# Optimization experiments

Hardware: AMD Instinct MI355X
Metric: run time of the kernel (lower is better)

## Reference

```python
import jax, jax.numpy as jnp
import numpy as np

C = 256
CK = C // 8  # key/query channels


def setup_inputs() -> dict:
    key = jax.random.key(0)
    ks = jax.random.split(key, 7)
    B, H, W = 8, 64, 64
    x = jax.random.normal(ks[0], (B, C, H, W), dtype=jnp.float32)
    # 1x1 conv weights (out_ch, in_ch) and biases. Spectral norm is a weight
    # reparameterization; at forward time it is just a conv with (normalized)
    # weights, so we sample weights directly.
    Wf = jax.random.normal(ks[1], (CK, C), dtype=jnp.float32) * 0.02
    bf = jnp.zeros((CK,), dtype=jnp.float32)
    Wg = jax.random.normal(ks[2], (CK, C), dtype=jnp.float32) * 0.02
    bg = jnp.zeros((CK,), dtype=jnp.float32)
    Wh = jax.random.normal(ks[3], (C, C), dtype=jnp.float32) * 0.02
    bh = jnp.zeros((C,), dtype=jnp.float32)
    gamma = jnp.ones((1,), dtype=jnp.float32) * 0.5  # nonzero so attention path matters
    return {"x": x, "Wf": Wf, "bf": bf, "Wg": Wg, "bg": bg, "Wh": Wh, "bh": bh, "gamma": gamma}


def reference(x, Wf, bf, Wg, bg, Wh, bh, gamma):
    b, c, h, w = x.shape
    n = h * w
    xf = x.reshape(b, c, n)  # [B, C, N]
    # 1x1 convs == per-pixel linear maps
    fx = jnp.einsum("kc,bcn->bkn", Wf, xf) + bf[None, :, None]  # [B, CK, N]
    gx = jnp.einsum("kc,bcn->bkn", Wg, xf) + bg[None, :, None]  # [B, CK, N]
    hx = jnp.einsum("oc,bcn->bon", Wh, xf) + bh[None, :, None]  # [B, C, N]
    # sx[b, i, j] = <fx[:, i], gx[:, j]>
    sx = jnp.einsum("bki,bkj->bij", fx, gx)  # [B, N, N]
    # torch F.softmax(sx, dim=1): normalize over the first N axis (i)
    beta = jax.nn.softmax(sx, axis=1)
    ox = jnp.einsum("bci,bij->bcj", hx, beta).reshape(b, c, h, w)
    return gamma.reshape(()) * ox + x
```

## Files before the change

kernel.cpp:

```cpp
#include <hip/hip_runtime.h>
#include <stdint.h>


typedef __bf16 bf16;
typedef __bf16 bf16x2 __attribute__((ext_vector_type(2)));
typedef __bf16 bf16x8 __attribute__((ext_vector_type(8)));
typedef float  f32x16 __attribute__((ext_vector_type(16)));
typedef float  f32x4  __attribute__((ext_vector_type(4)));
typedef unsigned char u8;
typedef long   i64;

#define BATCH 8
#define CC    256
#define CKK   32
#define NN    4096
#define LOG2E 1.4426950408889634f

__device__ __forceinline__ f32x16 zero16() {
  f32x16 z;
#pragma unroll
  for (int i = 0; i < 16; ++i) z[i] = 0.0f;
  return z;
}

__device__ __forceinline__ unsigned pack2(float lo, float hi) {
  bf16x2 v = {(bf16)lo, (bf16)hi};
  return __builtin_bit_cast(unsigned, v);
}

__device__ __forceinline__ f32x16 mfma32(bf16x8 a, bf16x8 b, f32x16 c) {
  return __builtin_amdgcn_mfma_f32_32x32x16_bf16(a, b, c, 0, 0, 0);
}

__device__ __forceinline__ f32x16 mfma8(i64 a, i64 b, f32x16 c) {
  return __builtin_amdgcn_mfma_f32_32x32x16_fp8_fp8(a, b, c, 0, 0, 0);
}

#define GLDS16(srcp, dstp)                                                         \
  __builtin_amdgcn_global_load_lds(                                               \
      (const __attribute__((address_space(1))) void*)(srcp),                      \
      (__attribute__((address_space(3))) void*)(dstp), 16, 0, 0)

__global__ __launch_bounds__(256) void k_transpose(const float* __restrict__ x,
                                                   bf16* __restrict__ xT) {
  __shared__ float tile[64][65];
  const int n0 = blockIdx.x * 64;
  const int c0 = blockIdx.y * 64;
  const int b  = blockIdx.z;
  const int t = threadIdx.x;
  const int tn = t & 63, trow = t >> 6;
#pragma unroll
  for (int i = 0; i < 16; ++i) {
    int c = trow + i * 4;
    tile[c][tn] = x[((size_t)(b * CC + c0 + c)) * NN + n0 + tn];
  }
  __syncthreads();
#pragma unroll
  for (int i = 0; i < 16; ++i) {
    int n = trow + i * 4;
    xT[((size_t)(b * NN + n0 + n)) * CC + c0 + tn] = (bf16)tile[tn][n];
  }
}

__global__ __launch_bounds__(64) void k_wprep(const float* __restrict__ Wf, const float* __restrict__ bfv,
                                              const float* __restrict__ Wg, const float* __restrict__ bg,
                                              const float* __restrict__ Wh, const float* __restrict__ bh,
                                              bf16* __restrict__ Wcat, float* __restrict__ bcat) {
  const int ko = blockIdx.x;
  const int t = threadIdx.x;
  const float* src;
  float scale = 1.0f;
  if (ko < 32) src = Wf + (size_t)ko * CC;
  else if (ko < 64) { src = Wg + (size_t)(ko - 32) * CC; scale = LOG2E; }
  else src = Wh + (size_t)(ko - 64) * CC;
#pragma unroll
  for (int i = 0; i < 4; ++i)
    Wcat[(size_t)ko * CC + t + i * 64] = (bf16)(src[t + i * 64] * scale);
  if (ko == 0) {
    for (int i = t; i < 320; i += 64) {
      float v = (i < 32) ? bfv[i] : (i < 64) ? bg[i - 32] * LOG2E : bh[i - 64];
      bcat[i] = v;
    }
  }
}

__global__ __launch_bounds__(256, 1) void k_proj(const bf16* __restrict__ xT,
                                                 const bf16* __restrict__ Wcat,
                                                 const float* __restrict__ bcat,
                                                 bf16* __restrict__ fxT, bf16* __restrict__ gxT,
                                                 u8* __restrict__ hx8) {
  const int d = blockIdx.x;
  const int b = d & 7, nb = d >> 3;
  const int t = threadIdx.x;
  const int w = t >> 6, ln = t & 63, ln31 = ln & 31, h = ln >> 5;
  const int n = nb * 128 + w * 32 + ln31;

  f32x16 acc[10];
#pragma unroll
  for (int mt = 0; mt < 10; ++mt) acc[mt] = zero16();

  const bf16* xrow = xT + ((size_t)(b * NN + n)) * CC;
#pragma unroll
  for (int ks = 0; ks < 16; ++ks) {
    bf16x8 bfrag = *(const bf16x8*)(xrow + ks * 16 + h * 8);
#pragma unroll
    for (int mt = 0; mt < 10; ++mt) {
      bf16x8 afrag = *(const bf16x8*)(Wcat + (size_t)(mt * 32 + ln31) * CC + ks * 16 + h * 8);
      acc[mt] = mfma32(afrag, bfrag, acc[mt]);
    }
  }

#pragma unroll
  for (int mt = 0; mt < 10; ++mt) {
#pragma unroll
    for (int q = 0; q < 4; ++q) {
      const int ko0 = mt * 32 + 8 * q + 4 * h;
      float v0 = acc[mt][4 * q + 0] + bcat[ko0 + 0];
      float v1 = acc[mt][4 * q + 1] + bcat[ko0 + 1];
      float v2 = acc[mt][4 * q + 2] + bcat[ko0 + 2];
      float v3 = acc[mt][4 * q + 3] + bcat[ko0 + 3];
      if (mt < 2) {
        bf16* dst = (mt == 0 ? fxT : gxT) + ((size_t)(b * NN + n)) * CKK + (8 * q + 4 * h);
        uint2 pv;
        pv.x = pack2(v0, v1);
        pv.y = pack2(v2, v3);
        *(uint2*)dst = pv;
      } else {
        const int c = ko0 - 64;
        unsigned wpk = (unsigned)__builtin_amdgcn_cvt_pk_fp8_f32(v0, v1, 0, false);
        wpk = (unsigned)__builtin_amdgcn_cvt_pk_fp8_f32(v2, v3, (int)wpk, true);
        u8* hp = hx8 + ((size_t)(b * CC + c)) * NN + n;
        hp[0]          = (u8)(wpk & 0xff);
        hp[NN]         = (u8)((wpk >> 8) & 0xff);
        hp[2 * NN]     = (u8)((wpk >> 16) & 0xff);
        hp[3 * NN]     = (u8)(wpk >> 24);
      }
    }
  }
}

__global__ __launch_bounds__(512, 2) void k_attn(const bf16* __restrict__ fxT,
                                                 const bf16* __restrict__ gxT,
                                                 const u8* __restrict__ hx8,
                                                 const float* __restrict__ x,
                                                 const float* __restrict__ gammap,
                                                 float* __restrict__ out) {
  extern __shared__ __align__(16) char smem[];
  __shared__ float lsh[128];
  const int d = blockIdx.x;
  const int b = d & 7, jb = d >> 3;
  const int t = threadIdx.x;
  const int g = t >> 8;
  const int tg = t & 255;
  const int wg = tg >> 6;
  const int ln = t & 63, ln31 = ln & 31, h = ln >> 5;
  const int j = jb * 128 + wg * 32 + ln31;
  const int kbase = g * 2048;

  const bf16* fxb = fxT + (size_t)b * NN * CKK;
  const u8*   hxb = hx8 + (size_t)b * CC * NN;

  u8*   vsg = (u8*)smem + g * 32768;
  bf16* ksg = (bf16*)(smem + 65536) + g * 6144;

  const bf16* qrow = gxT + ((size_t)b * NN + j) * CKK;
  bf16x8 qf0 = *(const bf16x8*)(qrow + h * 8);
  bf16x8 qf1 = *(const bf16x8*)(qrow + 16 + h * 8);
  asm volatile("" ::: "memory");

  int voff8[4];
#pragma unroll
  for (int ks = 0; ks < 4; ++ks)
    voff8[ks] = ln31 * 64 + (((ks + (ln31 >> 1)) & 3) * 16) + 8 * h;
  const int tk = (ln31 >> 1) & 3;
  const int ko0 = ln31 * 32 + ((h ^ tk) * 8);
  const int ko1 = ln31 * 32 + (((2 + h) ^ tk) * 8);

  const int vm = ((ln & 3) - (ln >> 3)) & 3;
  const u8* vlane8 = hxb + (size_t)(wg * 64 + (ln >> 2)) * NN + vm * 16;
  const int krow_l = ln >> 2;
  const int kcol_l = ((ln & 3) ^ ((ln >> 3) & 3)) * 8;
  const bf16* klane = fxb + (size_t)(wg * 16 + krow_l) * CKK + kcol_l;

#define STAGEV(slot, i0s)                                                     \
  {                                                                            \
    _Pragma("unroll")                                                          \
    for (int q = 0; q < 4; ++q)                                                \
      GLDS16(vlane8 + (size_t)q * 16 * NN + (i0s),                             \
             vsg + (slot) * 16384 + (wg * 4 + q) * 1024);                      \
  }
#define STAGEK(kslot, i0s)                                                    \
  { GLDS16(klane + (size_t)(i0s) * CKK, ksg + (kslot) * 2048 + wg * 16 * 32); }

  f32x16 oacc[8];
#pragma unroll
  for (int ct = 0; ct < 8; ++ct) oacc[ct] = zero16();
  float l_run = 0.0f;
  i64 pf[4] = {};

  auto QK = [&](int kslot, f32x16& s0, f32x16& s1) {
    const bf16* kt = ksg + kslot * 2048;
    bf16x8 kf00 = *(const bf16x8*)(kt + ko0);
    bf16x8 kf01 = *(const bf16x8*)(kt + ko1);
    bf16x8 kf10 = *(const bf16x8*)(kt + 1024 + ko0);
    bf16x8 kf11 = *(const bf16x8*)(kt + 1024 + ko1);
    s0 = zero16(); s1 = zero16();
    s0 = mfma32(kf00, qf0, s0);
    s0 = mfma32(kf01, qf1, s0);
    s1 = mfma32(kf10, qf0, s1);
    s1 = mfma32(kf11, qf1, s1);
  };
  auto SM = [&](const f32x16& s0, const f32x16& s1) {
    float e0[16], e1[16];
#pragma unroll
    for (int r = 0; r < 16; ++r) e0[r] = __builtin_exp2f(s0[r]);
#pragma unroll
    for (int r = 0; r < 16; ++r) e1[r] = __builtin_exp2f(s1[r]);
    float ls0 = 0.0f, ls1 = 0.0f, ls2 = 0.0f, ls3 = 0.0f;
#pragma unroll
    for (int r = 0; r < 4; ++r) {
      ls0 += e0[r];      ls1 += e0[4 + r];
      ls2 += e0[8 + r];  ls3 += e0[12 + r];
      ls0 += e1[r];      ls1 += e1[4 + r];
      ls2 += e1[8 + r];  ls3 += e1[12 + r];
    }
    l_run += (ls0 + ls1) + (ls2 + ls3);
    unsigned pk4[8];
#pragma unroll
    for (int A = 0; A < 4; ++A) {
      unsigned w = (unsigned)__builtin_amdgcn_cvt_pk_fp8_f32(e0[4 * A], e0[4 * A + 1], 0, false);
      pk4[A] = (unsigned)__builtin_amdgcn_cvt_pk_fp8_f32(e0[4 * A + 2], e0[4 * A + 3], (int)w, true);
    }
#pragma unroll
    for (int A = 0; A < 4; ++A) {
      unsigned w = (unsigned)__builtin_amdgcn_cvt_pk_fp8_f32(e1[4 * A], e1[4 * A + 1], 0, false);
      pk4[4 + A] = (unsigned)__builtin_amdgcn_cvt_pk_fp8_f32(e1[4 * A + 2], e1[4 * A + 3], (int)w, true);
    }
#pragma unroll
    for (int f = 0; f < 4; ++f) {
      unsigned xw = pk4[2 * f], yw = pk4[2 * f + 1];
      asm("v_permlane32_swap_b32 %0, %1" : "+v"(xw), "+v"(yw));
      pf[f] = (i64)(((unsigned long long)yw << 32) | xw);
    }
  };
  auto PV = [&](int slot) {
    const u8* vb = vsg + slot * 16384;
    i64 va0, va1, va2, va3, vn0, vn1, vn2, vn3;
    va0 = *(const i64*)(vb + voff8[0]);
    va1 = *(const i64*)(vb + voff8[1]);
    va2 = *(const i64*)(vb + voff8[2]);
    va3 = *(const i64*)(vb + voff8[3]);
    __builtin_amdgcn_s_setprio(1);
#pragma unroll
    for (int ct = 0; ct < 8; ++ct) {
      if (ct < 7) {
        const u8* vrow = vb + (ct + 1) * 2048;
        vn0 = *(const i64*)(vrow + voff8[0]);
        vn1 = *(const i64*)(vrow + voff8[1]);
        vn2 = *(const i64*)(vrow + voff8[2]);
        vn3 = *(const i64*)(vrow + voff8[3]);
      }
      oacc[ct] = mfma8(va0, pf[0], oacc[ct]);
      oacc[ct] = mfma8(va1, pf[1], oacc[ct]);
      oacc[ct] = mfma8(va2, pf[2], oacc[ct]);
      oacc[ct] = mfma8(va3, pf[3], oacc[ct]);
      va0 = vn0; va1 = vn1; va2 = vn2; va3 = vn3;
    }
    __builtin_amdgcn_s_setprio(0);
  };

  STAGEV(0, kbase);
  STAGEK(0, kbase);
  STAGEK(1, kbase + 64);

  for (int kb = 0; kb < 32; ++kb) {
    asm volatile("s_waitcnt vmcnt(0)" ::: "memory");
    __builtin_amdgcn_s_barrier();
    asm volatile("" ::: "memory");

    f32x16 s0, s1;
    if (g == 0) {
      QK(kb % 3, s0, s1);
      SM(s0, s1);
    } else if (kb > 0) {
      PV((kb - 1) & 1);
    }

    __builtin_amdgcn_s_barrier();
    asm volatile("" ::: "memory");

    STAGEV((kb + 1) & 1, kbase + ((kb + 1) & 31) * 64);
    STAGEK((kb + 2) % 3, kbase + ((kb + 2) & 31) * 64);

    if (g == 0) {
      PV(kb & 1);
    } else {
      QK(kb % 3, s0, s1);
      SM(s0, s1);
    }
  }
  if (g == 1) PV(31 & 1);

  l_run += __shfl_xor(l_run, 32);

  asm volatile("s_waitcnt vmcnt(0) lgkmcnt(0)" ::: "memory");
  __builtin_amdgcn_s_barrier();
  asm volatile("" ::: "memory");

  float* obuf = (float*)smem;
  const int jl = wg * 32 + ln31;
  if (g == 1) {
#pragma unroll
    for (int ct = 0; ct < 8; ++ct)
#pragma unroll
      for (int q = 0; q < 4; ++q) {
        f32x4 v;
        v[0] = oacc[ct][4 * q + 0];
        v[1] = oacc[ct][4 * q + 1];
        v[2] = oacc[ct][4 * q + 2];
        v[3] = oacc[ct][4 * q + 3];
        *(f32x4*)&obuf[jl * 260 + ct * 32 + 8 * q + 4 * h] = v;
      }
    if (h == 0) lsh[jl] = l_run;
  }
  __syncthreads();
  if (g == 0) {
    const float l = l_run + lsh[jl];
    const float ginv = gammap[0] / l;
    const float* xb = x + (size_t)b * CC * NN;
    float* ob = out + (size_t)b * CC * NN;
#pragma unroll
    for (int ct = 0; ct < 8; ++ct)
#pragma unroll
      for (int q = 0; q < 4; ++q) {
        f32x4 vB = *(const f32x4*)&obuf[jl * 260 + ct * 32 + 8 * q + 4 * h];
#pragma unroll
        for (int s = 0; s < 4; ++s) {
          int c = ct * 32 + 8 * q + 4 * h + s;
          size_t idx = (size_t)c * NN + j;
          float val = oacc[ct][4 * q + s] + vB[s];
          ob[idx] = fmaf(ginv, val, xb[idx]);
        }
      }
  }
#undef STAGEV
#undef STAGEK
}

extern "C" void kernel_launch(void* const* d_in, const int* in_sizes, int n_in,
                              void* d_out, int out_size, void* d_ws, size_t ws_size,
                              hipStream_t stream) {
  const float* x     = (const float*)d_in[0];
  const float* Wf    = (const float*)d_in[1];
  const float* bfv   = (const float*)d_in[2];
  const float* Wg    = (const float*)d_in[3];
  const float* bg    = (const float*)d_in[4];
  const float* Wh    = (const float*)d_in[5];
  const float* bh    = (const float*)d_in[6];
  const float* gamma = (const float*)d_in[7];
  float* out = (float*)d_out;

  char* ws = (char*)d_ws;
  bf16* fxT  = (bf16*)(ws);
  bf16* gxT  = (bf16*)(ws + 2097152);
  u8*   hx8  = (u8*)(ws + 4194304);
  bf16* Wcat = (bf16*)(ws + 12582912);
  float* bcat = (float*)(ws + 12746752);
  bf16* xT = (bf16*)d_out;

  k_transpose<<<dim3(64, 4, 8), 256, 0, stream>>>(x, xT);
  k_wprep<<<dim3(320), 64, 0, stream>>>(Wf, bfv, Wg, bg, Wh, bh, Wcat, bcat);
  k_proj<<<dim3(256), 256, 0, stream>>>(xT, Wcat, bcat, fxT, gxT, hx8);
  k_attn<<<dim3(256), 512, 133120, stream>>>(fxT, gxT, hx8, x, gamma, out);
}
```

Measured before the change: 136.4 us.

## Split projection across two blocks and relax attention load waits with deeper K ring

The projection kernel is split so each block computes half of the output channel tiles, doubling the grid and allowing two blocks per CU. This is meant to raise occupancy and parallelism for the projection. In the attention kernel the K staging ring goes from 3 to 4 slots, and the full vmcnt(0) wait becomes partial waits, letting the next tile's loads stay in flight across barriers. The setprio hints around PV and some zero initialization are also removed. The partial wait counts depend on the exact issue order of GLDS instructions, which risks reading data that has not landed yet.

```diff
diff --git a/kernel.cpp b/kernel.cpp
--- a/kernel.cpp
+++ b/kernel.cpp
@@ -84,41 +84,45 @@
   }
 }
 
-__global__ __launch_bounds__(256, 1) void k_proj(const bf16* __restrict__ xT,
+__global__ __launch_bounds__(256, 2) void k_proj(const bf16* __restrict__ xT,
                                                  const bf16* __restrict__ Wcat,
                                                  const float* __restrict__ bcat,
                                                  bf16* __restrict__ fxT, bf16* __restrict__ gxT,
                                                  u8* __restrict__ hx8) {
   const int d = blockIdx.x;
-  const int b = d & 7, nb = d >> 3;
+  const int half = d >> 8;
+  const int r = d & 255;
+  const int b = r & 7, nb = r >> 3;
   const int t = threadIdx.x;
   const int w = t >> 6, ln = t & 63, ln31 = ln & 31, h = ln >> 5;
   const int n = nb * 128 + w * 32 + ln31;
 
-  f32x16 acc[10];
-#pragma unroll
-  for (int mt = 0; mt < 10; ++mt) acc[mt] = zero16();
+  f32x16 acc[5];
+#pragma unroll
+  for (int m = 0; m < 5; ++m) acc[m] = zero16();
 
   const bf16* xrow = xT + ((size_t)(b * NN + n)) * CC;
 #pragma unroll
   for (int ks = 0; ks < 16; ++ks) {
     bf16x8 bfrag = *(const bf16x8*)(xrow + ks * 16 + h * 8);
 #pragma unroll
-    for (int mt = 0; mt < 10; ++mt) {
+    for (int m = 0; m < 5; ++m) {
+      const int mt = half * 5 + m;
       bf16x8 afrag = *(const bf16x8*)(Wcat + (size_t)(mt * 32 + ln31) * CC + ks * 16 + h * 8);
-      acc[mt] = mfma32(afrag, bfrag, acc[mt]);
-    }
-  }
-
-#pragma unroll
-  for (int mt = 0; mt < 10; ++mt) {
+      acc[m] = mfma32(afrag, bfrag, acc[m]);
+    }
+  }
+
+#pragma unroll
+  for (int m = 0; m < 5; ++m) {
+    const int mt = half * 5 + m;
 #pragma unroll
     for (int q = 0; q < 4; ++q) {
       const int ko0 = mt * 32 + 8 * q + 4 * h;
-      float v0 = acc[mt][4 * q + 0] + bcat[ko0 + 0];
-      float v1 = acc[mt][4 * q + 1] + bcat[ko0 + 1];
-      float v2 = acc[mt][4 * q + 2] + bcat[ko0 + 2];
-      float v3 = acc[mt][4 * q + 3] + bcat[ko0 + 3];
+      float v0 = acc[m][4 * q + 0] + bcat[ko0 + 0];
+      float v1 = acc[m][4 * q + 1] + bcat[ko0 + 1];
+      float v2 = acc[m][4 * q + 2] + bcat[ko0 + 2];
+      float v3 = acc[m][4 * q + 3] + bcat[ko0 + 3];
       if (mt < 2) {
         bf16* dst = (mt == 0 ? fxT : gxT) + ((size_t)(b * NN + n)) * CKK + (8 * q + 4 * h);
         uint2 pv;
@@ -130,10 +134,10 @@
         unsigned wpk = (unsigned)__builtin_amdgcn_cvt_pk_fp8_f32(v0, v1, 0, false);
         wpk = (unsigned)__builtin_amdgcn_cvt_pk_fp8_f32(v2, v3, (int)wpk, true);
         u8* hp = hx8 + ((size_t)(b * CC + c)) * NN + n;
-        hp[0]          = (u8)(wpk & 0xff);
-        hp[NN]         = (u8)((wpk >> 8) & 0xff);
-        hp[2 * NN]     = (u8)((wpk >> 16) & 0xff);
-        hp[3 * NN]     = (u8)(wpk >> 24);
+        hp[0]      = (u8)(wpk & 0xff);
+        hp[NN]     = (u8)((wpk >> 8) & 0xff);
+        hp[2 * NN] = (u8)((wpk >> 16) & 0xff);
+        hp[3 * NN] = (u8)(wpk >> 24);
       }
     }
   }
@@ -161,7 +165,7 @@
   const u8*   hxb = hx8 + (size_t)b * CC * NN;
 
   u8*   vsg = (u8*)smem + g * 32768;
-  bf16* ksg = (bf16*)(smem + 65536) + g * 6144;
+  bf16* ksg = (bf16*)(smem + 65536) + g * 8192;
 
   const bf16* qrow = gxT + ((size_t)b * NN + j) * CKK;
   bf16x8 qf0 = *(const bf16x8*)(qrow + h * 8);
@@ -190,11 +194,12 @@
              vsg + (slot) * 16384 + (wg * 4 + q) * 1024);                      \
   }
 #define STAGEK(kslot, i0s)                                                    \
-  { GLDS16(klane + (size_t)(i0s) * CKK, ksg + (kslot) * 2048 + wg * 16 * 32); }
+  { GLDS16(klane + (size_t)(i0s) * CKK, ksg + (kslot) * 2048 + wg * 512); }
 
   f32x16 oacc[8];
 #pragma unroll
   for (int ct = 0; ct < 8; ++ct) oacc[ct] = zero16();
+  const f32x16 vzero = zero16();
   float l_run = 0.0f;
   i64 pf[4] = {};
 
@@ -204,11 +209,8 @@
     bf16x8 kf01 = *(const bf16x8*)(kt + ko1);
     bf16x8 kf10 = *(const bf16x8*)(kt + 1024 + ko0);
     bf16x8 kf11 = *(const bf16x8*)(kt + 1024 + ko1);
-    s0 = zero16(); s1 = zero16();
-    s0 = mfma32(kf00, qf0, s0);
-    s0 = mfma32(kf01, qf1, s0);
-    s1 = mfma32(kf10, qf0, s1);
-    s1 = mfma32(kf11, qf1, s1);
+    s0 = mfma32(kf01, qf1, mfma32(kf00, qf0, vzero));
+    s1 = mfma32(kf11, qf1, mfma32(kf10, qf0, vzero));
   };
   auto SM = [&](const f32x16& s0, const f32x16& s1) {
     float e0[16], e1[16];
@@ -250,7 +252,6 @@
     va1 = *(const i64*)(vb + voff8[1]);
     va2 = *(const i64*)(vb + voff8[2]);
     va3 = *(const i64*)(vb + voff8[3]);
-    __builtin_amdgcn_s_setprio(1);
 #pragma unroll
     for (int ct = 0; ct < 8; ++ct) {
       if (ct < 7) {
@@ -266,36 +267,36 @@
       oacc[ct] = mfma8(va3, pf[3], oacc[ct]);
       va0 = vn0; va1 = vn1; va2 = vn2; va3 = vn3;
     }
-    __builtin_amdgcn_s_setprio(0);
   };
 
+  STAGEK(0, kbase);
   STAGEV(0, kbase);
-  STAGEK(0, kbase);
   STAGEK(1, kbase + 64);
 
   for (int kb = 0; kb < 32; ++kb) {
-    asm volatile("s_waitcnt vmcnt(0)" ::: "memory");
+    asm volatile("s_waitcnt vmcnt(5)" ::: "memory");
     __builtin_amdgcn_s_barrier();
     asm volatile("" ::: "memory");
 
     f32x16 s0, s1;
     if (g == 0) {
-      QK(kb % 3, s0, s1);
+      QK(kb & 3, s0, s1);
       SM(s0, s1);
     } else if (kb > 0) {
       PV((kb - 1) & 1);
     }
 
+    asm volatile("s_waitcnt vmcnt(1)" ::: "memory");
     __builtin_amdgcn_s_barrier();
     asm volatile("" ::: "memory");
 
     STAGEV((kb + 1) & 1, kbase + ((kb + 1) & 31) * 64);
-    STAGEK((kb + 2) % 3, kbase + ((kb + 2) & 31) * 64);
+    STAGEK((kb + 2) & 3, kbase + ((kb + 2) & 31) * 64);
 
     if (g == 0) {
       PV(kb & 1);
     } else {
-      QK(kb % 3, s0, s1);
+      QK(kb & 3, s0, s1);
       SM(s0, s1);
     }
   }
@@ -370,6 +371,6 @@
 
   k_transpose<<<dim3(64, 4, 8), 256, 0, stream>>>(x, xT);
   k_wprep<<<dim3(320), 64, 0, stream>>>(Wf, bfv, Wg, bg, Wh, bh, Wcat, bcat);
-  k_proj<<<dim3(256), 256, 0, stream>>>(xT, Wcat, bcat, fxT, gxT, hx8);
+  k_proj<<<dim3(512), 256, 0, stream>>>(xT, Wcat, bcat, fxT, gxT, hx8);
   k_attn<<<dim3(256), 512, 133120, stream>>>(fxT, gxT, hx8, x, gamma, out);
 }
```

New measurement: 120.9 us, median of 3. -11.4%, faster.
